# Performance work log

Hardware: AMD Instinct MI355X
Metric: run time of the kernel (lower is better)

## Reference

```python
import jax, jax.numpy as jnp
import numpy as np

N_QUBITS = 10
DIM = 2 ** N_QUBITS
N_POINTS = 64
D_FEAT = 10
N_LAYERS = 5

# bit tables: bits[:, q] = q-th least-significant bit of the state index.
# kron order in the original builds angles[n-1] x ... x angles[0], so angle q acts on bit q.
_bits = ((np.arange(DIM)[:, None] >> np.arange(N_QUBITS)[None, :]) & 1).astype(np.float32)
BITS_C = jnp.asarray(_bits - 0.5)  # (DIM, n): b_q - 1/2 -> rz diag phase coeffs
# crz ring: crz_matrix(i+1,...) is diagonal phase exp(i*theta*b_{i}*(b_{i+1}-1/2)) (control i, target i+1);
# close_ring is control n-1, target 0.
_ctrl = np.concatenate([np.arange(N_QUBITS - 1), [N_QUBITS - 1]])
_tgt = np.concatenate([np.arange(1, N_QUBITS), [0]])
RING_COEF = jnp.asarray(_bits[:, _ctrl] * (_bits[:, _tgt] - 0.5))  # (DIM, n)
H_GATES = jnp.broadcast_to(
    jnp.asarray((np.array([[1, 1], [1, -1]]) / np.sqrt(2)).astype(np.complex64)),
    (N_QUBITS, 2, 2))


def rz_diag(x, start):
    # rz_layer kron order: qubit q gets angle x[(start + n-1-q) % d]; rz = diag(e^{-it/2}, e^{it/2})
    idx = (start + N_QUBITS - 1 - np.arange(N_QUBITS)) % D_FEAT
    return jnp.exp(1j * (BITS_C @ x[idx]))  # (DIM,) complex64


def ring_diag(angles):
    return jnp.exp(1j * (RING_COEF @ angles))  # (DIM,) complex64


def ry_gates(angles):
    c, s = jnp.cos(0.5 * angles), jnp.sin(0.5 * angles)
    # (n, 2, 2): [[c, -s], [s, c]]
    return jnp.stack([jnp.stack([c, -s], -1), jnp.stack([s, c], -1)], -2).astype(jnp.complex64)


def apply_1q(state, gates):
    # apply gates[q] (2x2) to qubit q (axis n-1-q of the (2,)*n reshaped state)
    psi = state.reshape((2,) * N_QUBITS)
    for q in range(N_QUBITS):
        ax = N_QUBITS - 1 - q
        psi = jnp.moveaxis(jnp.tensordot(gates[q], psi, axes=([1], [ax])), 0, ax)
    return psi.reshape(DIM)


def block_f(state, x, bp, start):
    state = apply_1q(state, H_GATES)
    state = state * rz_diag(x, start)
    state = apply_1q(state, ry_gates(bp[0]))
    return state * ring_diag(bp[1])


def adj_block_f(state, x, bp, start):
    state = state * jnp.conj(ring_diag(bp[1]))
    state = apply_1q(state, ry_gates(-bp[0]))  # ry(t)^dagger = ry(-t)
    state = state * jnp.conj(rz_diag(x, start))
    return apply_1q(state, H_GATES)  # H is self-adjoint


def pair_prob(x1, x2, params):
    state = jnp.zeros((DIM,), jnp.complex64).at[0].set(1.0)
    for j in range(N_LAYERS):
        state = block_f(state, x1, params[j], j * N_QUBITS)
    for k in range(N_LAYERS):
        # faithful to original: start = (num_q - k - 1) * num_q (uses num_q, not n_layers)
        state = adj_block_f(state, x2, params[N_LAYERS - 1 - k], (N_QUBITS - k - 1) * N_QUBITS)
    a = state[0]
    return jnp.real(a) ** 2 + jnp.imag(a) ** 2  # |<0|U2^dag U1|0>|^2


def _kta(data, labels, params):
    x1 = jnp.repeat(data, N_POINTS, axis=0)   # point i of each pair
    x2 = jnp.tile(data, (N_POINTS, 1))        # point j of each pair
    k = jax.vmap(pair_prob, in_axes=(0, 0, None))(x1, x2, params)  # (N*N,)
    lm = (labels[:, None] * labels[None, :]).reshape(-1)
    kp = jnp.sum(lm * k)
    return kp / jnp.sqrt(jnp.sum(k * k) * jnp.sum(lm * lm))


def setup_inputs() -> dict:
    key = jax.random.key(0)
    k1, k2, k3 = jax.random.split(key, 3)
    data = jax.random.normal(k1, (N_POINTS, D_FEAT), jnp.float32)
    labels = jnp.where(jax.random.normal(k2, (N_POINTS,)) >= 0, 1.0, -1.0).astype(jnp.float32)
    params = jax.random.uniform(k3, (N_LAYERS, 2, N_QUBITS), jnp.float32, 0.0, 2.0 * np.pi)
    return {"data": data, "labels": labels, "params": params}


def reference(data, labels, params):
    return _kta(data, labels, params)
```

## Files before the change

kernel.cpp:

```cpp
#include <hip/hip_runtime.h>
#include <math.h>

#define NQ 10
#define DIM 1024
#define NPTS 64
#define DFEAT 10
#define NLAYERS 5
#define SREGS 4

#define IS2 0.70710678118654752440f

__global__ __launch_bounds__(256) void state_kernel(
    const float* __restrict__ data,
    const float* __restrict__ params,
    float2* __restrict__ psi)
{
    const int i    = blockIdx.x;
    const int tid  = threadIdx.x;
    const int lane = tid & 63;
    const int wv   = tid >> 6;

    __shared__ float4 mc[NLAYERS][NQ];
    __shared__ float2 xbuf[16][64];

    if (tid < NLAYERS * NQ) {
        const int L = tid / NQ, q = tid - L * NQ;
        const float xh = 0.5f * data[i * DFEAT + (9 - q)];
        const float cx = __cosf(xh), sx = __sinf(xh);
        float c = 1.f, s = 0.f;
        if (L != NLAYERS - 1) {
            const float th = 0.5f * params[L * 2 * NQ + q];
            c = __cosf(th); s = __sinf(th);
        }
        const float p = (c + s) * IS2, qm = (c - s) * IS2;
        mc[L][q] = make_float4(qm * cx, -p * sx, p * cx, -qm * sx);
    }
    __syncthreads();

    float re[SREGS], im[SREGS];
#pragma unroll
    for (int r = 0; r < SREGS; ++r) { re[r] = 0.f; im[r] = 0.f; }
    if (tid == 0) re[0] = 1.f;

#pragma unroll 1
    for (int L = 0; L < NLAYERS; ++L) {

#pragma unroll 1
        for (int q = 0; q < 6; ++q) {
            const float4 m = mc[L][q];
            const int   b = (lane >> q) & 1;
            const float msr = b ? -m.x : m.x;
            const float msi = m.y;
            const float mpr = m.z;
            const float mpi = b ? -m.w : m.w;
            float pr[SREGS], pi[SREGS];
#pragma unroll
            for (int r = 0; r < SREGS; ++r) {
                pr[r] = __shfl_xor(re[r], 1 << q, 64);
                pi[r] = __shfl_xor(im[r], 1 << q, 64);
            }
#pragma unroll
            for (int r = 0; r < SREGS; ++r) {
                const float nr = msr * re[r] - msi * im[r] + mpr * pr[r] - mpi * pi[r];
                const float ni = msr * im[r] + msi * re[r] + mpr * pi[r] + mpi * pr[r];
                re[r] = nr; im[r] = ni;
            }
        }

#pragma unroll 1
        for (int q = 6; q < 8; ++q) {
            const float4 m = mc[L][q];
            const int   b = (wv >> (q - 6)) & 1;
            const float msr = b ? -m.x : m.x;
            const float msi = m.y;
            const float mpr = m.z;
            const float mpi = b ? -m.w : m.w;
#pragma unroll
            for (int r = 0; r < SREGS; ++r)
                xbuf[(wv << 2) | r][lane] = make_float2(re[r], im[r]);
            __syncthreads();
            const int pw = wv ^ (1 << (q - 6));
#pragma unroll
            for (int r = 0; r < SREGS; ++r) {
                const float2 p2 = xbuf[(pw << 2) | r][lane];
                const float nr = msr * re[r] - msi * im[r] + mpr * p2.x - mpi * p2.y;
                const float ni = msr * im[r] + msi * re[r] + mpr * p2.y + mpi * p2.x;
                re[r] = nr; im[r] = ni;
            }
            __syncthreads();
        }

#pragma unroll
        for (int q = 8; q < 10; ++q) {
            const int mask = 1 << (q - 8);
            const float4 m = mc[L][q];
            const float m00r = m.x, m00i = m.y, m01r = m.z, m01i = m.w;
            const float m10r = m.z, m10i = -m.w, m11r = -m.x, m11i = m.y;
#pragma unroll
            for (int r = 0; r < SREGS; ++r) {
                if (!(r & mask)) {
                    const int r1 = r | mask;
                    const float a0r = re[r],  a0i = im[r];
                    const float a1r = re[r1], a1i = im[r1];
                    re[r]  = m00r * a0r - m00i * a0i + m01r * a1r - m01i * a1i;
                    im[r]  = m00r * a0i + m00i * a0r + m01r * a1i + m01i * a1r;
                    re[r1] = m10r * a0r - m10i * a0i + m11r * a1r - m11i * a1i;
                    im[r1] = m10r * a0i + m10i * a0r + m11r * a1i + m11i * a1r;
                }
            }
        }

        if (L < NLAYERS - 1) {
            const float* rg = params + L * 2 * NQ + NQ;
            float ph[SREGS] = {0.f, 0.f, 0.f, 0.f};
#pragma unroll 1
            for (int n = 0; n < NQ; ++n) {
                const int   nn = (n == 9) ? 0 : (n + 1);
                const float g  = rg[n];
#pragma unroll
                for (int r = 0; r < SREGS; ++r) {
                    const int idx = (r << 8) | (wv << 6) | lane;
                    const float t = (((idx >> nn) & 1) ? 0.5f : -0.5f) * g;
                    ph[r] += ((idx >> n) & 1) ? t : 0.f;
                }
            }
#pragma unroll
            for (int r = 0; r < SREGS; ++r) {
                const float s = __sinf(ph[r]), c = __cosf(ph[r]);
                const float nr = re[r] * c - im[r] * s;
                const float ni = re[r] * s + im[r] * c;
                re[r] = nr; im[r] = ni;
            }
        }
    }

    float2* out = psi + i * DIM;
#pragma unroll
    for (int r = 0; r < SREGS; ++r)
        out[(r << 8) | (wv << 6) | lane] = make_float2(re[r], im[r]);
}

__global__ __launch_bounds__(256) void gram_kernel(
    const float4* __restrict__ psi4,
    float* __restrict__ Kbuf)
{
    const int wave = threadIdx.x >> 6;
    const int lane = threadIdx.x & 63;
    const int p    = blockIdx.x * 4 + wave;
    const int i    = p >> 6;
    const int j    = p & 63;
    if (j < i) return;

    const float4* a = psi4 + i * (DIM / 2);
    const float4* b = psi4 + j * (DIM / 2);

    float zr = 0.f, zi = 0.f;
#pragma unroll
    for (int r = 0; r < 8; ++r) {
        const int k = (r << 6) | lane;
        float4 av = a[k], bv = b[k];
        zr += bv.x * av.x + bv.y * av.y + bv.z * av.z + bv.w * av.w;
        zi += bv.x * av.y - bv.y * av.x + bv.z * av.w - bv.w * av.z;
    }
#pragma unroll
    for (int off = 32; off; off >>= 1) {
        zr += __shfl_xor(zr, off, 64);
        zi += __shfl_xor(zi, off, 64);
    }
    if (lane == 0) {
        const float k = zr * zr + zi * zi;
        Kbuf[p] = k;
        Kbuf[(j << 6) | i] = k;
    }
}

__global__ __launch_bounds__(256) void reduce_kernel(
    const float* __restrict__ Kbuf,
    const float* __restrict__ labels,
    float* __restrict__ out)
{
    __shared__ float sm[3][4];
    const int tid  = threadIdx.x;
    const int lane = tid & 63;
    const int wave = tid >> 6;

    float slk = 0.f, skk = 0.f, sll = 0.f;
#pragma unroll
    for (int it = 0; it < (NPTS * NPTS) / 256; ++it) {
        const int p = it * 256 + tid;
        const float K  = Kbuf[p];
        const float lm = labels[p >> 6] * labels[p & 63];
        slk += lm * K;
        skk += K * K;
        sll += lm * lm;
    }
#pragma unroll
    for (int off = 32; off; off >>= 1) {
        slk += __shfl_xor(slk, off, 64);
        skk += __shfl_xor(skk, off, 64);
        sll += __shfl_xor(sll, off, 64);
    }
    if (lane == 0) { sm[0][wave] = slk; sm[1][wave] = skk; sm[2][wave] = sll; }
    __syncthreads();
    if (tid == 0) {
        float a = sm[0][0] + sm[0][1] + sm[0][2] + sm[0][3];
        float b = sm[1][0] + sm[1][1] + sm[1][2] + sm[1][3];
        float c = sm[2][0] + sm[2][1] + sm[2][2] + sm[2][3];
        out[0] = a / sqrtf(b * c);
    }
}

extern "C" void kernel_launch(void* const* d_in, const int* in_sizes, int n_in,
                              void* d_out, int out_size, void* d_ws, size_t ws_size,
                              hipStream_t stream) {
    const float* data   = (const float*)d_in[0];
    const float* labels = (const float*)d_in[1];
    const float* params = (const float*)d_in[2];
    float* out = (float*)d_out;

    float2* psi  = (float2*)d_ws;
    float*  Kbuf = (float*)((char*)d_ws + (size_t)NPTS * DIM * sizeof(float2));

    state_kernel <<<NPTS,            256, 0, stream>>>(data, params, psi);
    gram_kernel  <<<NPTS * NPTS / 4, 256, 0, stream>>>((const float4*)psi, Kbuf);
    reduce_kernel<<<1,               256, 0, stream>>>(Kbuf, labels, out);
}
```

Baseline: 75.82 us.

## Fuse KTA reduction into gram kernel and start from analytic product state

The separate reduce kernel is removed. Each gram block now folds its weighted K and K^2 contributions into bucketed global atomics, and a last-block ticket computes the final alignment, which saves one launch and the Kbuf round-trip. The first layer's single-qubit gates are applied analytically to |0>, since the result is a product state, which skips the shuffle and shared-memory passes for that layer. The change relies on atomics and a ticket counter that are zeroed in the state kernel. It also uses sum(lm^2) = (sum l^2)^2, and floating-point summation order now varies between runs.

```diff
diff --git a/kernel.cpp b/kernel.cpp
--- a/kernel.cpp
+++ b/kernel.cpp
@@ -7,18 +7,24 @@
 #define DFEAT 10
 #define NLAYERS 5
 #define SREGS 4
+#define NBUCKET 16
 
 #define IS2 0.70710678118654752440f
+
+#define ACC_OFF ((size_t)NPTS * DIM * sizeof(float2))
 
 __global__ __launch_bounds__(256) void state_kernel(
     const float* __restrict__ data,
     const float* __restrict__ params,
-    float2* __restrict__ psi)
+    float2* __restrict__ psi,
+    float* __restrict__ acc)
 {
     const int i    = blockIdx.x;
     const int tid  = threadIdx.x;
     const int lane = tid & 63;
     const int wv   = tid >> 6;
+
+    if (i == 0 && tid < 2 * NBUCKET + 1) acc[tid] = 0.f;
 
     __shared__ float4 mc[NLAYERS][NQ];
     __shared__ float2 xbuf[16][64];
@@ -38,74 +44,97 @@
     __syncthreads();
 
     float re[SREGS], im[SREGS];
-#pragma unroll
-    for (int r = 0; r < SREGS; ++r) { re[r] = 0.f; im[r] = 0.f; }
-    if (tid == 0) re[0] = 1.f;
+
+    {
+        float Pr = 1.f, Pi = 0.f;
+#pragma unroll 1
+        for (int q = 0; q < 8; ++q) {
+            const float4 m = mc[0][q];
+            const int b = (q < 6) ? ((lane >> q) & 1) : ((wv >> (q - 6)) & 1);
+            const float fr = b ? m.z : m.x;
+            const float fi = b ? -m.w : m.y;
+            const float nr = Pr * fr - Pi * fi;
+            const float ni = Pr * fi + Pi * fr;
+            Pr = nr; Pi = ni;
+        }
+        const float4 m8 = mc[0][8], m9 = mc[0][9];
+        const float u8r[2] = {m8.x, m8.z},  u8i[2] = {m8.y, -m8.w};
+        const float u9r[2] = {m9.x, m9.z},  u9i[2] = {m9.y, -m9.w};
+#pragma unroll
+        for (int r = 0; r < SREGS; ++r) {
+            const int b8 = r & 1, b9 = (r >> 1) & 1;
+            const float vr = u8r[b8] * u9r[b9] - u8i[b8] * u9i[b9];
+            const float vi = u8r[b8] * u9i[b9] + u8i[b8] * u9r[b9];
+            re[r] = Pr * vr - Pi * vi;
+            im[r] = Pr * vi + Pi * vr;
+        }
+    }
 
 #pragma unroll 1
     for (int L = 0; L < NLAYERS; ++L) {
-
-#pragma unroll 1
-        for (int q = 0; q < 6; ++q) {
-            const float4 m = mc[L][q];
-            const int   b = (lane >> q) & 1;
-            const float msr = b ? -m.x : m.x;
-            const float msi = m.y;
-            const float mpr = m.z;
-            const float mpi = b ? -m.w : m.w;
-            float pr[SREGS], pi[SREGS];
-#pragma unroll
-            for (int r = 0; r < SREGS; ++r) {
-                pr[r] = __shfl_xor(re[r], 1 << q, 64);
-                pi[r] = __shfl_xor(im[r], 1 << q, 64);
-            }
-#pragma unroll
-            for (int r = 0; r < SREGS; ++r) {
-                const float nr = msr * re[r] - msi * im[r] + mpr * pr[r] - mpi * pi[r];
-                const float ni = msr * im[r] + msi * re[r] + mpr * pi[r] + mpi * pr[r];
-                re[r] = nr; im[r] = ni;
-            }
-        }
-
-#pragma unroll 1
-        for (int q = 6; q < 8; ++q) {
-            const float4 m = mc[L][q];
-            const int   b = (wv >> (q - 6)) & 1;
-            const float msr = b ? -m.x : m.x;
-            const float msi = m.y;
-            const float mpr = m.z;
-            const float mpi = b ? -m.w : m.w;
-#pragma unroll
-            for (int r = 0; r < SREGS; ++r)
-                xbuf[(wv << 2) | r][lane] = make_float2(re[r], im[r]);
-            __syncthreads();
-            const int pw = wv ^ (1 << (q - 6));
-#pragma unroll
-            for (int r = 0; r < SREGS; ++r) {
-                const float2 p2 = xbuf[(pw << 2) | r][lane];
-                const float nr = msr * re[r] - msi * im[r] + mpr * p2.x - mpi * p2.y;
-                const float ni = msr * im[r] + msi * re[r] + mpr * p2.y + mpi * p2.x;
-                re[r] = nr; im[r] = ni;
-            }
-            __syncthreads();
-        }
-
-#pragma unroll
-        for (int q = 8; q < 10; ++q) {
-            const int mask = 1 << (q - 8);
-            const float4 m = mc[L][q];
-            const float m00r = m.x, m00i = m.y, m01r = m.z, m01i = m.w;
-            const float m10r = m.z, m10i = -m.w, m11r = -m.x, m11i = m.y;
-#pragma unroll
-            for (int r = 0; r < SREGS; ++r) {
-                if (!(r & mask)) {
-                    const int r1 = r | mask;
-                    const float a0r = re[r],  a0i = im[r];
-                    const float a1r = re[r1], a1i = im[r1];
-                    re[r]  = m00r * a0r - m00i * a0i + m01r * a1r - m01i * a1i;
-                    im[r]  = m00r * a0i + m00i * a0r + m01r * a1i + m01i * a1r;
-                    re[r1] = m10r * a0r - m10i * a0i + m11r * a1r - m11i * a1i;
-                    im[r1] = m10r * a0i + m10i * a0r + m11r * a1i + m11i * a1r;
+        if (L > 0) {
+#pragma unroll 1
+            for (int q = 0; q < 6; ++q) {
+                const float4 m = mc[L][q];
+                const int   b = (lane >> q) & 1;
+                const float msr = b ? -m.x : m.x;
+                const float msi = m.y;
+                const float mpr = m.z;
+                const float mpi = b ? -m.w : m.w;
+                float pr[SREGS], pi[SREGS];
+#pragma unroll
+                for (int r = 0; r < SREGS; ++r) {
+                    pr[r] = __shfl_xor(re[r], 1 << q, 64);
+                    pi[r] = __shfl_xor(im[r], 1 << q, 64);
+                }
+#pragma unroll
+                for (int r = 0; r < SREGS; ++r) {
+                    const float nr = msr * re[r] - msi * im[r] + mpr * pr[r] - mpi * pi[r];
+                    const float ni = msr * im[r] + msi * re[r] + mpr * pi[r] + mpi * pr[r];
+                    re[r] = nr; im[r] = ni;
+                }
+            }
+
+#pragma unroll 1
+            for (int q = 6; q < 8; ++q) {
+                const float4 m = mc[L][q];
+                const int   b = (wv >> (q - 6)) & 1;
+                const float msr = b ? -m.x : m.x;
+                const float msi = m.y;
+                const float mpr = m.z;
+                const float mpi = b ? -m.w : m.w;
+#pragma unroll
+                for (int r = 0; r < SREGS; ++r)
+                    xbuf[(wv << 2) | r][lane] = make_float2(re[r], im[r]);
+                __syncthreads();
+                const int pw = wv ^ (1 << (q - 6));
+#pragma unroll
+                for (int r = 0; r < SREGS; ++r) {
+                    const float2 p2 = xbuf[(pw << 2) | r][lane];
+                    const float nr = msr * re[r] - msi * im[r] + mpr * p2.x - mpi * p2.y;
+                    const float ni = msr * im[r] + msi * re[r] + mpr * p2.y + mpi * p2.x;
+                    re[r] = nr; im[r] = ni;
+                }
+                __syncthreads();
+            }
+
+#pragma unroll
+            for (int q = 8; q < 10; ++q) {
+                const int mask = 1 << (q - 8);
+                const float4 m = mc[L][q];
+                const float m00r = m.x, m00i = m.y, m01r = m.z, m01i = m.w;
+                const float m10r = m.z, m10i = -m.w, m11r = -m.x, m11i = m.y;
+#pragma unroll
+                for (int r = 0; r < SREGS; ++r) {
+                    if (!(r & mask)) {
+                        const int r1 = r | mask;
+                        const float a0r = re[r],  a0i = im[r];
+                        const float a1r = re[r1], a1i = im[r1];
+                        re[r]  = m00r * a0r - m00i * a0i + m01r * a1r - m01i * a1i;
+                        im[r]  = m00r * a0i + m00i * a0r + m01r * a1i + m01i * a1r;
+                        re[r1] = m10r * a0r - m10i * a0i + m11r * a1r - m11i * a1i;
+                        im[r1] = m10r * a0i + m10i * a0r + m11r * a1i + m11i * a1r;
+                    }
                 }
             }
         }
@@ -142,71 +171,62 @@
 
 __global__ __launch_bounds__(256) void gram_kernel(
     const float4* __restrict__ psi4,
-    float* __restrict__ Kbuf)
+    const float* __restrict__ labels,
+    float* __restrict__ acc,
+    float* __restrict__ out)
 {
+    __shared__ float sm[2][4];
     const int wave = threadIdx.x >> 6;
     const int lane = threadIdx.x & 63;
     const int p    = blockIdx.x * 4 + wave;
     const int i    = p >> 6;
     const int j    = p & 63;
-    if (j < i) return;
-
-    const float4* a = psi4 + i * (DIM / 2);
-    const float4* b = psi4 + j * (DIM / 2);
-
-    float zr = 0.f, zi = 0.f;
-#pragma unroll
-    for (int r = 0; r < 8; ++r) {
-        const int k = (r << 6) | lane;
-        float4 av = a[k], bv = b[k];
-        zr += bv.x * av.x + bv.y * av.y + bv.z * av.z + bv.w * av.w;
-        zi += bv.x * av.y - bv.y * av.x + bv.z * av.w - bv.w * av.z;
-    }
-#pragma unroll
-    for (int off = 32; off; off >>= 1) {
-        zr += __shfl_xor(zr, off, 64);
-        zi += __shfl_xor(zi, off, 64);
-    }
-    if (lane == 0) {
+
+    float slk_w = 0.f, skk_w = 0.f;
+    if (j >= i) {
+        const float4* a = psi4 + i * (DIM / 2);
+        const float4* b = psi4 + j * (DIM / 2);
+        float zr = 0.f, zi = 0.f;
+#pragma unroll
+        for (int r = 0; r < 8; ++r) {
+            const int k = (r << 6) | lane;
+            float4 av = a[k], bv = b[k];
+            zr += bv.x * av.x + bv.y * av.y + bv.z * av.z + bv.w * av.w;
+            zi += bv.x * av.y - bv.y * av.x + bv.z * av.w - bv.w * av.z;
+        }
+#pragma unroll
+        for (int off = 32; off; off >>= 1) {
+            zr += __shfl_xor(zr, off, 64);
+            zi += __shfl_xor(zi, off, 64);
+        }
         const float k = zr * zr + zi * zi;
-        Kbuf[p] = k;
-        Kbuf[(j << 6) | i] = k;
-    }
-}
-
-__global__ __launch_bounds__(256) void reduce_kernel(
-    const float* __restrict__ Kbuf,
-    const float* __restrict__ labels,
-    float* __restrict__ out)
-{
-    __shared__ float sm[3][4];
-    const int tid  = threadIdx.x;
-    const int lane = tid & 63;
-    const int wave = tid >> 6;
-
-    float slk = 0.f, skk = 0.f, sll = 0.f;
-#pragma unroll
-    for (int it = 0; it < (NPTS * NPTS) / 256; ++it) {
-        const int p = it * 256 + tid;
-        const float K  = Kbuf[p];
-        const float lm = labels[p >> 6] * labels[p & 63];
-        slk += lm * K;
-        skk += K * K;
-        sll += lm * lm;
-    }
-#pragma unroll
-    for (int off = 32; off; off >>= 1) {
-        slk += __shfl_xor(slk, off, 64);
-        skk += __shfl_xor(skk, off, 64);
-        sll += __shfl_xor(sll, off, 64);
-    }
-    if (lane == 0) { sm[0][wave] = slk; sm[1][wave] = skk; sm[2][wave] = sll; }
+        const float w = (i == j) ? 1.f : 2.f;
+        slk_w = w * labels[i] * labels[j] * k;
+        skk_w = w * k * k;
+    }
+    if (lane == 0) { sm[0][wave] = slk_w; sm[1][wave] = skk_w; }
     __syncthreads();
-    if (tid == 0) {
-        float a = sm[0][0] + sm[0][1] + sm[0][2] + sm[0][3];
-        float b = sm[1][0] + sm[1][1] + sm[1][2] + sm[1][3];
-        float c = sm[2][0] + sm[2][1] + sm[2][2] + sm[2][3];
-        out[0] = a / sqrtf(b * c);
+
+    if (threadIdx.x == 0) {
+        const float bs = sm[0][0] + sm[0][1] + sm[0][2] + sm[0][3];
+        const float bk = sm[1][0] + sm[1][1] + sm[1][2] + sm[1][3];
+        const int bkt = blockIdx.x & (NBUCKET - 1);
+        atomicAdd(&acc[bkt], bs);
+        atomicAdd(&acc[NBUCKET + bkt], bk);
+        __threadfence();
+        unsigned* ticket = (unsigned*)(acc + 2 * NBUCKET);
+        const unsigned t = atomicAdd(ticket, 1u);
+        if (t == (unsigned)(gridDim.x - 1)) {
+            float slk = 0.f, skk = 0.f;
+#pragma unroll
+            for (int q = 0; q < NBUCKET; ++q) {
+                slk += atomicAdd(&acc[q], 0.f);
+                skk += atomicAdd(&acc[NBUCKET + q], 0.f);
+            }
+            float sl2 = 0.f;
+            for (int q = 0; q < NPTS; ++q) { const float l = labels[q]; sl2 += l * l; }
+            out[0] = slk / sqrtf(skk * (sl2 * sl2));
+        }
     }
 }
 
@@ -218,10 +238,9 @@
     const float* params = (const float*)d_in[2];
     float* out = (float*)d_out;
 
-    float2* psi  = (float2*)d_ws;
-    float*  Kbuf = (float*)((char*)d_ws + (size_t)NPTS * DIM * sizeof(float2));
-
-    state_kernel <<<NPTS,            256, 0, stream>>>(data, params, psi);
-    gram_kernel  <<<NPTS * NPTS / 4, 256, 0, stream>>>((const float4*)psi, Kbuf);
-    reduce_kernel<<<1,               256, 0, stream>>>(Kbuf, labels, out);
+    float2* psi = (float2*)d_ws;
+    float*  acc = (float*)((char*)d_ws + ACC_OFF);
+
+    state_kernel<<<NPTS,            256, 0, stream>>>(data, params, psi, acc);
+    gram_kernel <<<NPTS * NPTS / 4, 256, 0, stream>>>((const float4*)psi, labels, acc, out);
 }
```

Measured after the change: 103.2 us. 36.0% more time.

## Use one thread per amplitude, analytic first layer, and upper-triangle gram with block partials

Applied to the files above, without the earlier changes.

The state kernel now runs 1024 threads per point, one amplitude each, and uses LDS exchange for qubits 6-9. Layer 0 is computed as a closed-form product state instead of applying gates to |0>. The gram kernel launches only the 2080 upper-triangle pairs, using a sqrt-based index mapping. Each block folds the label-weighted sums into per-block partials, which removes the full K matrix write and the idle waves. The label norm is computed as (sum l^2)^2, and the cost is more block-wide barriers per layer in the state kernel.

```diff
diff --git a/kernel.cpp b/kernel.cpp
--- a/kernel.cpp
+++ b/kernel.cpp
@@ -6,11 +6,14 @@
 #define NPTS 64
 #define DFEAT 10
 #define NLAYERS 5
-#define SREGS 4
+#define NPAIR 2080
+#define GBLK  (NPAIR / 4)
 
 #define IS2 0.70710678118654752440f
 
-__global__ __launch_bounds__(256) void state_kernel(
+#define PART_OFF ((size_t)NPTS * DIM * sizeof(float2))
+
+__global__ __launch_bounds__(1024) void state_kernel(
     const float* __restrict__ data,
     const float* __restrict__ params,
     float2* __restrict__ psi)
@@ -18,10 +21,9 @@
     const int i    = blockIdx.x;
     const int tid  = threadIdx.x;
     const int lane = tid & 63;
-    const int wv   = tid >> 6;
 
     __shared__ float4 mc[NLAYERS][NQ];
-    __shared__ float2 xbuf[16][64];
+    __shared__ float2 xbuf[DIM];
 
     if (tid < NLAYERS * NQ) {
         const int L = tid / NQ, q = tid - L * NQ;
@@ -37,119 +39,92 @@
     }
     __syncthreads();
 
-    float re[SREGS], im[SREGS];
-#pragma unroll
-    for (int r = 0; r < SREGS; ++r) { re[r] = 0.f; im[r] = 0.f; }
-    if (tid == 0) re[0] = 1.f;
+    float re, im;
+    {
+        float Pr = 1.f, Pi = 0.f;
+#pragma unroll 1
+        for (int q = 0; q < NQ; ++q) {
+            const float4 m = mc[0][q];
+            const int b = (tid >> q) & 1;
+            const float fr = b ? m.z : m.x;
+            const float fi = b ? -m.w : m.y;
+            const float nr = Pr * fr - Pi * fi;
+            const float ni = Pr * fi + Pi * fr;
+            Pr = nr; Pi = ni;
+        }
+        re = Pr; im = Pi;
+    }
 
 #pragma unroll 1
     for (int L = 0; L < NLAYERS; ++L) {
-
-#pragma unroll 1
-        for (int q = 0; q < 6; ++q) {
-            const float4 m = mc[L][q];
-            const int   b = (lane >> q) & 1;
-            const float msr = b ? -m.x : m.x;
-            const float msi = m.y;
-            const float mpr = m.z;
-            const float mpi = b ? -m.w : m.w;
-            float pr[SREGS], pi[SREGS];
-#pragma unroll
-            for (int r = 0; r < SREGS; ++r) {
-                pr[r] = __shfl_xor(re[r], 1 << q, 64);
-                pi[r] = __shfl_xor(im[r], 1 << q, 64);
+        if (L > 0) {
+#pragma unroll 1
+            for (int q = 0; q < 6; ++q) {
+                const float4 m = mc[L][q];
+                const int   b = (lane >> q) & 1;
+                const float msr = b ? -m.x : m.x;
+                const float msi = m.y;
+                const float mpr = m.z;
+                const float mpi = b ? -m.w : m.w;
+                const float pr = __shfl_xor(re, 1 << q, 64);
+                const float pi = __shfl_xor(im, 1 << q, 64);
+                const float nr = msr * re - msi * im + mpr * pr - mpi * pi;
+                const float ni = msr * im + msi * re + mpr * pi + mpi * pr;
+                re = nr; im = ni;
             }
-#pragma unroll
-            for (int r = 0; r < SREGS; ++r) {
-                const float nr = msr * re[r] - msi * im[r] + mpr * pr[r] - mpi * pi[r];
-                const float ni = msr * im[r] + msi * re[r] + mpr * pi[r] + mpi * pr[r];
-                re[r] = nr; im[r] = ni;
-            }
-        }
-
-#pragma unroll 1
-        for (int q = 6; q < 8; ++q) {
-            const float4 m = mc[L][q];
-            const int   b = (wv >> (q - 6)) & 1;
-            const float msr = b ? -m.x : m.x;
-            const float msi = m.y;
-            const float mpr = m.z;
-            const float mpi = b ? -m.w : m.w;
-#pragma unroll
-            for (int r = 0; r < SREGS; ++r)
-                xbuf[(wv << 2) | r][lane] = make_float2(re[r], im[r]);
-            __syncthreads();
-            const int pw = wv ^ (1 << (q - 6));
-#pragma unroll
-            for (int r = 0; r < SREGS; ++r) {
-                const float2 p2 = xbuf[(pw << 2) | r][lane];
-                const float nr = msr * re[r] - msi * im[r] + mpr * p2.x - mpi * p2.y;
-                const float ni = msr * im[r] + msi * re[r] + mpr * p2.y + mpi * p2.x;
-                re[r] = nr; im[r] = ni;
-            }
-            __syncthreads();
-        }
-
-#pragma unroll
-        for (int q = 8; q < 10; ++q) {
-            const int mask = 1 << (q - 8);
-            const float4 m = mc[L][q];
-            const float m00r = m.x, m00i = m.y, m01r = m.z, m01i = m.w;
-            const float m10r = m.z, m10i = -m.w, m11r = -m.x, m11i = m.y;
-#pragma unroll
-            for (int r = 0; r < SREGS; ++r) {
-                if (!(r & mask)) {
-                    const int r1 = r | mask;
-                    const float a0r = re[r],  a0i = im[r];
-                    const float a1r = re[r1], a1i = im[r1];
-                    re[r]  = m00r * a0r - m00i * a0i + m01r * a1r - m01i * a1i;
-                    im[r]  = m00r * a0i + m00i * a0r + m01r * a1i + m01i * a1r;
-                    re[r1] = m10r * a0r - m10i * a0i + m11r * a1r - m11i * a1i;
-                    im[r1] = m10r * a0i + m10i * a0r + m11r * a1i + m11i * a1r;
-                }
+#pragma unroll 1
+            for (int q = 6; q < NQ; ++q) {
+                const float4 m = mc[L][q];
+                const int   b = (tid >> q) & 1;
+                const float msr = b ? -m.x : m.x;
+                const float msi = m.y;
+                const float mpr = m.z;
+                const float mpi = b ? -m.w : m.w;
+                xbuf[tid] = make_float2(re, im);
+                __syncthreads();
+                const float2 p2 = xbuf[tid ^ (1 << q)];
+                const float nr = msr * re - msi * im + mpr * p2.x - mpi * p2.y;
+                const float ni = msr * im + msi * re + mpr * p2.y + mpi * p2.x;
+                re = nr; im = ni;
+                __syncthreads();
             }
         }
 
         if (L < NLAYERS - 1) {
             const float* rg = params + L * 2 * NQ + NQ;
-            float ph[SREGS] = {0.f, 0.f, 0.f, 0.f};
+            float ph = 0.f;
 #pragma unroll 1
             for (int n = 0; n < NQ; ++n) {
                 const int   nn = (n == 9) ? 0 : (n + 1);
                 const float g  = rg[n];
-#pragma unroll
-                for (int r = 0; r < SREGS; ++r) {
-                    const int idx = (r << 8) | (wv << 6) | lane;
-                    const float t = (((idx >> nn) & 1) ? 0.5f : -0.5f) * g;
-                    ph[r] += ((idx >> n) & 1) ? t : 0.f;
-                }
+                const float t  = (((tid >> nn) & 1) ? 0.5f : -0.5f) * g;
+                ph += ((tid >> n) & 1) ? t : 0.f;
             }
-#pragma unroll
-            for (int r = 0; r < SREGS; ++r) {
-                const float s = __sinf(ph[r]), c = __cosf(ph[r]);
-                const float nr = re[r] * c - im[r] * s;
-                const float ni = re[r] * s + im[r] * c;
-                re[r] = nr; im[r] = ni;
-            }
-        }
-    }
-
-    float2* out = psi + i * DIM;
-#pragma unroll
-    for (int r = 0; r < SREGS; ++r)
-        out[(r << 8) | (wv << 6) | lane] = make_float2(re[r], im[r]);
+            const float s = __sinf(ph), c = __cosf(ph);
+            const float nr = re * c - im * s;
+            const float ni = re * s + im * c;
+            re = nr; im = ni;
+        }
+    }
+
+    psi[i * DIM + tid] = make_float2(re, im);
 }
 
 __global__ __launch_bounds__(256) void gram_kernel(
     const float4* __restrict__ psi4,
-    float* __restrict__ Kbuf)
+    const float* __restrict__ labels,
+    float* __restrict__ partials)
 {
+    __shared__ float sm[2][4];
     const int wave = threadIdx.x >> 6;
     const int lane = threadIdx.x & 63;
-    const int p    = blockIdx.x * 4 + wave;
-    const int i    = p >> 6;
-    const int j    = p & 63;
-    if (j < i) return;
+    const int w    = blockIdx.x * 4 + wave;
+
+    int i = (int)((129.0f - sqrtf(16641.0f - 8.0f * (float)w)) * 0.5f);
+    int Ci = 64 * i - ((i * (i - 1)) >> 1);
+    while (w < Ci)            { --i; Ci = 64 * i - ((i * (i - 1)) >> 1); }
+    while (w >= Ci + 64 - i)  { Ci += 64 - i; ++i; }
+    const int j = i + (w - Ci);
 
     const float4* a = psi4 + i * (DIM / 2);
     const float4* b = psi4 + j * (DIM / 2);
@@ -158,7 +133,7 @@
 #pragma unroll
     for (int r = 0; r < 8; ++r) {
         const int k = (r << 6) | lane;
-        float4 av = a[k], bv = b[k];
+        const float4 av = a[k], bv = b[k];
         zr += bv.x * av.x + bv.y * av.y + bv.z * av.z + bv.w * av.w;
         zi += bv.x * av.y - bv.y * av.x + bv.z * av.w - bv.w * av.z;
     }
@@ -167,15 +142,22 @@
         zr += __shfl_xor(zr, off, 64);
         zi += __shfl_xor(zi, off, 64);
     }
+
     if (lane == 0) {
         const float k = zr * zr + zi * zi;
-        Kbuf[p] = k;
-        Kbuf[(j << 6) | i] = k;
+        const float wgt = (i == j) ? 1.f : 2.f;
+        sm[0][wave] = wgt * labels[i] * labels[j] * k;
+        sm[1][wave] = wgt * k * k;
+    }
+    __syncthreads();
+    if (threadIdx.x == 0) {
+        partials[2 * blockIdx.x]     = sm[0][0] + sm[0][1] + sm[0][2] + sm[0][3];
+        partials[2 * blockIdx.x + 1] = sm[1][0] + sm[1][1] + sm[1][2] + sm[1][3];
     }
 }
 
 __global__ __launch_bounds__(256) void reduce_kernel(
-    const float* __restrict__ Kbuf,
+    const float* __restrict__ partials,
     const float* __restrict__ labels,
     float* __restrict__ out)
 {
@@ -184,29 +166,26 @@
     const int lane = tid & 63;
     const int wave = tid >> 6;
 
-    float slk = 0.f, skk = 0.f, sll = 0.f;
-#pragma unroll
-    for (int it = 0; it < (NPTS * NPTS) / 256; ++it) {
-        const int p = it * 256 + tid;
-        const float K  = Kbuf[p];
-        const float lm = labels[p >> 6] * labels[p & 63];
-        slk += lm * K;
-        skk += K * K;
-        sll += lm * lm;
-    }
+    float slk = 0.f, skk = 0.f, sl2 = 0.f;
+    for (int p = tid; p < GBLK; p += 256) {
+        slk += partials[2 * p];
+        skk += partials[2 * p + 1];
+    }
+    if (tid < NPTS) { const float l = labels[tid]; sl2 = l * l; }
+
 #pragma unroll
     for (int off = 32; off; off >>= 1) {
         slk += __shfl_xor(slk, off, 64);
         skk += __shfl_xor(skk, off, 64);
-        sll += __shfl_xor(sll, off, 64);
-    }
-    if (lane == 0) { sm[0][wave] = slk; sm[1][wave] = skk; sm[2][wave] = sll; }
+        sl2 += __shfl_xor(sl2, off, 64);
+    }
+    if (lane == 0) { sm[0][wave] = slk; sm[1][wave] = skk; sm[2][wave] = sl2; }
     __syncthreads();
     if (tid == 0) {
-        float a = sm[0][0] + sm[0][1] + sm[0][2] + sm[0][3];
-        float b = sm[1][0] + sm[1][1] + sm[1][2] + sm[1][3];
-        float c = sm[2][0] + sm[2][1] + sm[2][2] + sm[2][3];
-        out[0] = a / sqrtf(b * c);
+        const float a = sm[0][0] + sm[0][1] + sm[0][2] + sm[0][3];
+        const float b = sm[1][0] + sm[1][1] + sm[1][2] + sm[1][3];
+        const float c = sm[2][0] + sm[2][1] + sm[2][2] + sm[2][3];
+        out[0] = a / sqrtf(b * (c * c));
     }
 }
 
@@ -218,10 +197,10 @@
     const float* params = (const float*)d_in[2];
     float* out = (float*)d_out;
 
-    float2* psi  = (float2*)d_ws;
-    float*  Kbuf = (float*)((char*)d_ws + (size_t)NPTS * DIM * sizeof(float2));
-
-    state_kernel <<<NPTS,            256, 0, stream>>>(data, params, psi);
-    gram_kernel  <<<NPTS * NPTS / 4, 256, 0, stream>>>((const float4*)psi, Kbuf);
-    reduce_kernel<<<1,               256, 0, stream>>>(Kbuf, labels, out);
-}
+    float2* psi      = (float2*)d_ws;
+    float*  partials = (float*)((char*)d_ws + PART_OFF);
+
+    state_kernel <<<NPTS, 1024, 0, stream>>>(data, params, psi);
+    gram_kernel  <<<GBLK,  256, 0, stream>>>((const float4*)psi, labels, partials);
+    reduce_kernel<<<1,     256, 0, stream>>>(partials, labels, out);
+}
```

Result: faster. 73.89 us (-2.5%).
